# Kernel optimization log

Hardware: AMD Instinct MI355X
Metric: run time of the kernel (lower is better)

Reference implementation:

```python
import jax, jax.numpy as jnp
import numpy as np

B, S, D, H = 2, 2048, 1024, 16
HD = D // H  # head dim = 64


def setup_inputs() -> dict:
    key = jax.random.key(0)
    k1, k2, k3, k4 = jax.random.split(key, 4)
    x = jax.random.normal(k1, (B, S, D), dtype=jnp.float32)
    context = jax.random.normal(k2, (B, S, D), dtype=jnp.float32)
    Wq = jax.random.normal(k3, (D, D), dtype=jnp.float32) * 0.02   # to_query weight [out,in]
    Wkv = jax.random.normal(k4, (2 * D, D), dtype=jnp.float32) * 0.02  # to_key_value weight [out,in]
    return {"x": x, "context": context, "Wq": Wq, "Wkv": Wkv}


def reference(x, context, Wq, Wkv):
    b, i, _ = x.shape
    j = context.shape[1]
    # projections (torch Linear: y = x @ W.T)
    q = x @ Wq.T                      # [b, i, D]
    kv = context @ Wkv.T              # [b, j, 2D]
    k, v = kv[..., :D], kv[..., D:]
    # split heads: (h c) ordering -> reshape last dim to [H, HD]
    q = q.reshape(b, i, H, HD).transpose(0, 2, 1, 3)  # [b,h,i,c]
    k = k.reshape(b, j, H, HD).transpose(0, 2, 1, 3)  # [b,h,j,c]
    v = v.reshape(b, j, H, HD).transpose(0, 2, 1, 3)  # [b,h,j,c]
    q = q * (HD ** -0.5)
    scores = jnp.einsum('bhic,bhjc->bhij', q, k)      # [b,h,i,j]
    scores = scores - jax.lax.stop_gradient(scores.max(axis=-1, keepdims=True))
    attn = jax.nn.softmax(scores, axis=-1)
    out = jnp.einsum('bhij,bhjc->bhic', attn, v)      # [b,h,i,c]
    out = out.transpose(0, 2, 1, 3).reshape(b, i, H * HD)  # 'b h n d -> b n (h d)'
    return out
```

## Files before the change

### kernel.cpp

```cpp
#include <hip/hip_runtime.h>
#include <hip/hip_bf16.h>
#include <stdint.h>

typedef unsigned short u16;
typedef __attribute__((ext_vector_type(8))) __bf16 bf16x8;
typedef __attribute__((ext_vector_type(4))) float f32x4;
typedef __attribute__((ext_vector_type(16))) float f32x16;

#define AS1(p) ((const __attribute__((address_space(1))) void*)(p))
#define AS3(p) ((__attribute__((address_space(3))) void*)(p))

__device__ __forceinline__ u16 f2bf(float f) {
  union { float f; uint32_t u; } c; c.f = f;
  uint32_t u = c.u;
  u += 0x7fffu + ((u >> 16) & 1u);
  return (u16)(u >> 16);
}

__device__ __forceinline__ float exp2_fast(float x) {
  float r; asm("v_exp_f32 %0, %1" : "=v"(r) : "v"(x)); return r;
}

__global__ __launch_bounds__(256) void cast4_f32_bf16(
    const float4* __restrict__ s0, ushort4* __restrict__ d0, int n0,
    const float4* __restrict__ s1, ushort4* __restrict__ d1, int n1,
    const float4* __restrict__ s2, ushort4* __restrict__ d2, int n2,
    const float4* __restrict__ s3, ushort4* __restrict__ d3, int n3) {
  int bid = blockIdx.x;
  const float4* src; ushort4* dst; int n4, b0, nb;
  if (bid < 512)       { src = s0; dst = d0; n4 = n0; b0 = 0;    nb = 512; }
  else if (bid < 1024) { src = s1; dst = d1; n4 = n1; b0 = 512;  nb = 512; }
  else if (bid < 1152) { src = s2; dst = d2; n4 = n2; b0 = 1024; nb = 128; }
  else                 { src = s3; dst = d3; n4 = n3; b0 = 1152; nb = 256; }
  int stride = nb * 256;
  for (int i = (bid - b0) * 256 + threadIdx.x; i < n4; i += stride) {
    float4 v = src[i];
    ushort4 o;
    o.x = f2bf(v.x); o.y = f2bf(v.y); o.z = f2bf(v.z); o.w = f2bf(v.w);
    dst[i] = o;
  }
}

__global__ __launch_bounds__(256) void gemm_fused(const u16* __restrict__ xb,
                                                  const u16* __restrict__ wqb,
                                                  u16* __restrict__ qo,
                                                  const u16* __restrict__ cb,
                                                  const u16* __restrict__ wkb,
                                                  u16* __restrict__ kvo,
                                                  float scale_q) {
  __shared__ u16 As[2][128 * 32];
  __shared__ u16 Bs[2][128 * 32];
  const int K = 1024;
  int bid = blockIdx.x;
  const u16 *A, *B; u16* C; int N, bm, bn; float scale;
  if (bid < 256) { A = xb; B = wqb; C = qo;  N = 1024; bm = bid >> 3; bn = bid & 7;  scale = scale_q; }
  else { int b2 = bid - 256; A = cb; B = wkb; C = kvo; N = 2048; bm = b2 >> 4; bn = b2 & 15; scale = 1.0f; }

  int tid = threadIdx.x;
  int w = tid >> 6, l = tid & 63;
  int wr = w >> 1, wc = w & 1;
  int lr = l & 15, lg = l >> 4;

  const u16* Abase = A + (size_t)(bm * 128 + (l >> 2)) * K + (l & 3) * 8;
  const u16* Bbase = B + (size_t)(bn * 128 + (l >> 2)) * K + (l & 3) * 8;

  f32x4 acc[4][4];
#pragma unroll
  for (int i = 0; i < 4; ++i)
#pragma unroll
    for (int j = 0; j < 4; ++j) acc[i][j] = (f32x4){0.f, 0.f, 0.f, 0.f};

#define STAGE(buf, k0)                                                              \
  {                                                                                 \
    _Pragma("unroll")                                                               \
    for (int t2 = 0; t2 < 2; ++t2) {                                                \
      int seg = w * 2 + t2;                                                         \
      __builtin_amdgcn_global_load_lds(AS1(Abase + (size_t)seg * 16 * K + (k0)),    \
                                       AS3(&As[buf][seg * 512]), 16, 0, 0);         \
      __builtin_amdgcn_global_load_lds(AS1(Bbase + (size_t)seg * 16 * K + (k0)),    \
                                       AS3(&Bs[buf][seg * 512]), 16, 0, 0);         \
    }                                                                               \
  }

  STAGE(0, 0);
  for (int t = 0; t < 32; ++t) {
    int cur = t & 1;
    if (t < 31) {
      STAGE(cur ^ 1, (t + 1) * 32);
      asm volatile("s_waitcnt vmcnt(4)" ::: "memory");
    } else {
      asm volatile("s_waitcnt vmcnt(0)" ::: "memory");
    }
    __builtin_amdgcn_s_barrier();
    bf16x8 af[4], bb[4];
#pragma unroll
    for (int i = 0; i < 4; ++i)
      af[i] = *(const bf16x8*)(&As[cur][(wr * 64 + i * 16 + lr) * 32 + lg * 8]);
#pragma unroll
    for (int j = 0; j < 4; ++j)
      bb[j] = *(const bf16x8*)(&Bs[cur][(wc * 64 + j * 16 + lr) * 32 + lg * 8]);
    asm volatile("s_waitcnt lgkmcnt(0)" ::: "memory");
    __builtin_amdgcn_sched_barrier(0);
#pragma unroll
    for (int i = 0; i < 4; ++i)
#pragma unroll
      for (int j = 0; j < 4; ++j)
        acc[i][j] = __builtin_amdgcn_mfma_f32_16x16x32_bf16(af[i], bb[j], acc[i][j], 0, 0, 0);
    __builtin_amdgcn_s_barrier();
  }
#undef STAGE

#pragma unroll
  for (int i = 0; i < 4; ++i)
#pragma unroll
    for (int j = 0; j < 4; ++j)
#pragma unroll
      for (int r = 0; r < 4; ++r) {
        int row = bm * 128 + wr * 64 + i * 16 + lg * 4 + r;
        int col = bn * 128 + wc * 64 + j * 16 + lr;
        C[(size_t)row * N + col] = f2bf(acc[i][j][r] * scale);
      }
}

#define SQ 2048
#define NT 32

__global__ __launch_bounds__(256, 2) void attn_kernel(const u16* __restrict__ Q,
                                                      const u16* __restrict__ KV,
                                                      float* __restrict__ O) {
  __shared__ u16 Ks[2 * 64 * 64];
  __shared__ u16 Vt[2 * 64 * 64];

  int qt = blockIdx.x & 15;
  int bh = blockIdx.x >> 4;
  int b = bh >> 4, h = bh & 15;
  int tid = threadIdx.x;
  int w = tid >> 6, l = tid & 63;
  int li = l & 31, hi = l >> 5;
  int jr = l >> 3, bk = l & 7;

  const u16* kbase = KV + (size_t)b * SQ * 2048 + (size_t)h * 64;
  const u16* vbase = kbase + 1024;
  int i0g = qt * 128 + w * 32;
  const u16* qrow = Q + (size_t)(b * SQ + i0g + li) * 1024 + h * 64;

  bf16x8 qf0 = *(const bf16x8*)(qrow + 0  + hi * 8);
  bf16x8 qf1 = *(const bf16x8*)(qrow + 16 + hi * 8);
  bf16x8 qf2 = *(const bf16x8*)(qrow + 32 + hi * 8);
  bf16x8 qf3 = *(const bf16x8*)(qrow + 48 + hi * 8);

  {
    const u16* gk0 = kbase + (size_t)(w * 8 + jr) * 2048 + ((bk ^ jr) * 8);
    __builtin_amdgcn_global_load_lds(AS1(gk0), AS3(Ks + w * 512), 16, 0, 0);
    const u16* gk1 = kbase + (size_t)(32 + w * 8 + jr) * 2048 + ((bk ^ jr) * 8);
    __builtin_amdgcn_global_load_lds(AS1(gk1), AS3(Ks + 2048 + w * 512), 16, 0, 0);
  }
  uint4 vregA = *(const uint4*)(vbase + (size_t)(tid >> 3) * 2048 + (tid & 7) * 8);
  uint4 vregB = *(const uint4*)(vbase + (size_t)(32 + (tid >> 3)) * 2048 + (tid & 7) * 8);

  float m_run = -1e30f, l_run = 0.f;
  f32x16 acc0, acc1;
#pragma unroll
  for (int r = 0; r < 16; ++r) { acc0[r] = 0.f; acc1[r] = 0.f; }

  auto stage_pf = [&](int t) {
    u16* Vtc = Vt + (t & 1) * 4096;
    int a = tid & 7, jj0 = tid >> 3;
    const u16* pa_ = (const u16*)&vregA;
#pragma unroll
    for (int e = 0; e < 8; ++e)
      *(u16*)((char*)Vtc + (a * 8 + e) * 128 + ((jj0 * 2) ^ ((e ^ a) << 4))) = pa_[e];
    const u16* pb_ = (const u16*)&vregB;
    int jj1 = 32 + jj0;
#pragma unroll
    for (int e = 0; e < 8; ++e)
      *(u16*)((char*)Vtc + (a * 8 + e) * 128 + ((jj1 * 2) ^ ((e ^ a) << 4))) = pb_[e];
    if (t + 1 < NT) {
      int j0n = (t + 1) * 64;
      u16* Ksn = Ks + ((t + 1) & 1) * 4096;
      const u16* gk0 = kbase + (size_t)(j0n + w * 8 + jr) * 2048 + ((bk ^ jr) * 8);
      __builtin_amdgcn_global_load_lds(AS1(gk0), AS3(Ksn + w * 512), 16, 0, 0);
      const u16* gk1 = kbase + (size_t)(j0n + 32 + w * 8 + jr) * 2048 + ((bk ^ jr) * 8);
      __builtin_amdgcn_global_load_lds(AS1(gk1), AS3(Ksn + 2048 + w * 512), 16, 0, 0);
      vregA = *(const uint4*)(vbase + (size_t)(j0n + (tid >> 3)) * 2048 + (tid & 7) * 8);
      vregB = *(const uint4*)(vbase + (size_t)(j0n + 32 + (tid >> 3)) * 2048 + (tid & 7) * 8);
    }
  };

  auto qkt = [&](int t, f32x16& n0, f32x16& n1) {
    const u16* Ksc = Ks + (t & 1) * 4096;
#pragma unroll
    for (int r = 0; r < 16; ++r) { n0[r] = 0.f; n1[r] = 0.f; }
    int swk = (li & 7) << 4;
    __builtin_amdgcn_s_setprio(1);
#pragma unroll
    for (int kb = 0; kb < 4; ++kb) {
      bf16x8 k0 = *(const bf16x8*)((const char*)Ksc + li * 128        + ((kb * 32 + hi * 16) ^ swk));
      bf16x8 k1 = *(const bf16x8*)((const char*)Ksc + (32 + li) * 128 + ((kb * 32 + hi * 16) ^ swk));
      bf16x8 qq = (kb == 0) ? qf0 : (kb == 1) ? qf1 : (kb == 2) ? qf2 : qf3;
      n0 = __builtin_amdgcn_mfma_f32_32x32x16_bf16(k0, qq, n0, 0, 0, 0);
      n1 = __builtin_amdgcn_mfma_f32_32x32x16_bf16(k1, qq, n1, 0, 0, 0);
    }
    __builtin_amdgcn_s_setprio(0);
  };

  auto finish_pv = [&](int tp, const f32x16& sp0, const f32x16& sp1) {
    const u16* Vtp = Vt + (tp & 1) * 4096;
    float p0[16], p1[16];
    float sum = 0.f;
#pragma unroll
    for (int r = 0; r < 16; ++r) { p0[r] = exp2_fast(sp0[r] - m_run); sum += p0[r]; }
#pragma unroll
    for (int r = 0; r < 16; ++r) { p1[r] = exp2_fast(sp1[r] - m_run); sum += p1[r]; }
    sum += __shfl_xor(sum, 32);
    l_run += sum;
    unsigned pw[16];
#pragma unroll
    for (int i2 = 0; i2 < 8; ++i2) {
      asm("v_cvt_pk_bf16_f32 %0, %1, %2" : "=v"(pw[i2])     : "v"(p0[2 * i2]), "v"(p0[2 * i2 + 1]));
      asm("v_cvt_pk_bf16_f32 %0, %1, %2" : "=v"(pw[8 + i2]) : "v"(p1[2 * i2]), "v"(p1[2 * i2 + 1]));
    }
#pragma unroll
    for (int gB = 0; gB < 2; ++gB) {
      int o = gB * 8;
      asm volatile("v_permlane32_swap_b32 %0, %1" : "+v"(pw[o + 0]), "+v"(pw[o + 2]));
      asm volatile("v_permlane32_swap_b32 %0, %1" : "+v"(pw[o + 1]), "+v"(pw[o + 3]));
      asm volatile("v_permlane32_swap_b32 %0, %1" : "+v"(pw[o + 4]), "+v"(pw[o + 6]));
      asm volatile("v_permlane32_swap_b32 %0, %1" : "+v"(pw[o + 5]), "+v"(pw[o + 7]));
    }
    __builtin_amdgcn_s_setprio(1);
#pragma unroll
    for (int kb2 = 0; kb2 < 4; ++kb2) {
      uint4 ufr;
      ufr.x = pw[kb2 * 4 + 0]; ufr.y = pw[kb2 * 4 + 1];
      ufr.z = pw[kb2 * 4 + 2]; ufr.w = pw[kb2 * 4 + 3];
      bf16x8 pa = *(bf16x8*)&ufr;
      int jbyte = kb2 * 32 + hi * 16;
      int d0_ = li, d1_ = 32 + li;
      bf16x8 v0 = *(const bf16x8*)((const char*)Vtp + d0_ * 128 + (jbyte ^ (((d0_ ^ (d0_ >> 3)) & 7) << 4)));
      bf16x8 v1 = *(const bf16x8*)((const char*)Vtp + d1_ * 128 + (jbyte ^ (((d1_ ^ (d1_ >> 3)) & 7) << 4)));
      acc0 = __builtin_amdgcn_mfma_f32_32x32x16_bf16(v0, pa, acc0, 0, 0, 0);
      acc1 = __builtin_amdgcn_mfma_f32_32x32x16_bf16(v1, pa, acc1, 0, 0, 0);
    }
    __builtin_amdgcn_s_setprio(0);
  };

  auto maxred = [&](const f32x16& n0, const f32x16& n1) {
    float pm = fmaxf(n0[0], n0[1]);
#pragma unroll
    for (int r = 2; r < 16; r += 2) pm = fmaxf(fmaxf(pm, n0[r]), n0[r + 1]);
#pragma unroll
    for (int r = 0; r < 16; r += 2) pm = fmaxf(fmaxf(pm, n1[r]), n1[r + 1]);
    pm = fmaxf(pm, __shfl_xor(pm, 32));
    if (!__all(pm <= m_run + 8.0f)) {
      float mnew = fmaxf(m_run, pm);
      float esc = exp2_fast(m_run - mnew);
      m_run = mnew;
      l_run *= esc;
#pragma unroll
      for (int r = 0; r < 16; ++r) { acc0[r] *= esc; acc1[r] *= esc; }
    }
  };

  f32x16 sa0, sa1, sb0, sb1;
  __syncthreads();
  stage_pf(0);
  qkt(0, sa0, sa1);
  maxred(sa0, sa1);
  for (int t = 1; t < NT - 1; t += 2) {
    __syncthreads();
    stage_pf(t);
    qkt(t, sb0, sb1);
    finish_pv(t - 1, sa0, sa1);
    maxred(sb0, sb1);
    __syncthreads();
    stage_pf(t + 1);
    qkt(t + 1, sa0, sa1);
    finish_pv(t, sb0, sb1);
    maxred(sa0, sa1);
  }
  __syncthreads();
  stage_pf(NT - 1);
  qkt(NT - 1, sb0, sb1);
  finish_pv(NT - 2, sa0, sa1);
  maxred(sb0, sb1);
  __syncthreads();
  finish_pv(NT - 1, sb0, sb1);

  float inv = 1.f / l_run;
  float* orow = O + ((size_t)(b * SQ + i0g + li) * 1024 + h * 64);
#pragma unroll
  for (int g = 0; g < 4; ++g) {
    f32x4 o0, o1;
#pragma unroll
    for (int q_ = 0; q_ < 4; ++q_) {
      o0[q_] = acc0[g * 4 + q_] * inv;
      o1[q_] = acc1[g * 4 + q_] * inv;
    }
    *(f32x4*)(orow + 8 * g + 4 * hi) = o0;
    *(f32x4*)(orow + 32 + 8 * g + 4 * hi) = o1;
  }
}

extern "C" void kernel_launch(void* const* d_in, const int* in_sizes, int n_in,
                              void* d_out, int out_size, void* d_ws, size_t ws_size,
                              hipStream_t stream) {
  (void)in_sizes; (void)n_in; (void)out_size; (void)ws_size;
  const float* x   = (const float*)d_in[0];
  const float* ctx = (const float*)d_in[1];
  const float* Wq  = (const float*)d_in[2];
  const float* Wkv = (const float*)d_in[3];
  float* out = (float*)d_out;
  char* ws = (char*)d_ws;

  u16* xb  = (u16*)(ws);
  u16* cb  = (u16*)(ws + (8ull  << 20));
  u16* wqb = (u16*)(ws + (16ull << 20));
  u16* wkb = (u16*)(ws + (18ull << 20));
  u16* q   = (u16*)(ws + (22ull << 20));
  u16* kv  = (u16*)(ws + (30ull << 20));

  cast4_f32_bf16<<<1408, 256, 0, stream>>>(
      (const float4*)x,   (ushort4*)xb,  (4096 * 1024) / 4,
      (const float4*)ctx, (ushort4*)cb,  (4096 * 1024) / 4,
      (const float4*)Wq,  (ushort4*)wqb, (1024 * 1024) / 4,
      (const float4*)Wkv, (ushort4*)wkb, (2048 * 1024) / 4);

  gemm_fused<<<768, 256, 0, stream>>>(xb, wqb, q, cb, wkb, kv, 0.125f * 1.44269504f);

  attn_kernel<<<512, 256, 0, stream>>>(q, kv, out);
}
```

Before: 110.9 us.

## Fuse fp32-to-bf16 cast into projection GEMM and drop the cast kernel

Removes the separate cast kernel. The GEMM now loads fp32 activations and weights directly into registers, converts them with packed bf16 conversion instructions and writes them to a swizzled LDS layout. The next tile is prefetched in registers instead of using async global-to-LDS loads. This saves one launch and a write/read round trip of the bf16 copies. In exchange each GEMM tile reads twice the bytes, and weights are reconverted in every block, with register pressure raised by the occupancy hint of 3.

```diff
diff --git a/kernel.cpp b/kernel.cpp
--- a/kernel.cpp
+++ b/kernel.cpp
@@ -21,48 +21,36 @@
   float r; asm("v_exp_f32 %0, %1" : "=v"(r) : "v"(x)); return r;
 }
 
-__global__ __launch_bounds__(256) void cast4_f32_bf16(
-    const float4* __restrict__ s0, ushort4* __restrict__ d0, int n0,
-    const float4* __restrict__ s1, ushort4* __restrict__ d1, int n1,
-    const float4* __restrict__ s2, ushort4* __restrict__ d2, int n2,
-    const float4* __restrict__ s3, ushort4* __restrict__ d3, int n3) {
-  int bid = blockIdx.x;
-  const float4* src; ushort4* dst; int n4, b0, nb;
-  if (bid < 512)       { src = s0; dst = d0; n4 = n0; b0 = 0;    nb = 512; }
-  else if (bid < 1024) { src = s1; dst = d1; n4 = n1; b0 = 512;  nb = 512; }
-  else if (bid < 1152) { src = s2; dst = d2; n4 = n2; b0 = 1024; nb = 128; }
-  else                 { src = s3; dst = d3; n4 = n3; b0 = 1152; nb = 256; }
-  int stride = nb * 256;
-  for (int i = (bid - b0) * 256 + threadIdx.x; i < n4; i += stride) {
-    float4 v = src[i];
-    ushort4 o;
-    o.x = f2bf(v.x); o.y = f2bf(v.y); o.z = f2bf(v.z); o.w = f2bf(v.w);
-    dst[i] = o;
-  }
-}
-
-__global__ __launch_bounds__(256) void gemm_fused(const u16* __restrict__ xb,
-                                                  const u16* __restrict__ wqb,
-                                                  u16* __restrict__ qo,
-                                                  const u16* __restrict__ cb,
-                                                  const u16* __restrict__ wkb,
-                                                  u16* __restrict__ kvo,
-                                                  float scale_q) {
+__device__ __forceinline__ unsigned pkbf(float lo, float hi) {
+  unsigned r;
+  asm("v_cvt_pk_bf16_f32 %0, %1, %2" : "=v"(r) : "v"(lo), "v"(hi));
+  return r;
+}
+
+__global__ __launch_bounds__(256, 3) void gemm_fused(const float* __restrict__ xf,
+                                                     const float* __restrict__ wqf,
+                                                     u16* __restrict__ qo,
+                                                     const float* __restrict__ cf,
+                                                     const float* __restrict__ wkf,
+                                                     u16* __restrict__ kvo,
+                                                     float scale_q) {
   __shared__ u16 As[2][128 * 32];
   __shared__ u16 Bs[2][128 * 32];
   const int K = 1024;
   int bid = blockIdx.x;
-  const u16 *A, *B; u16* C; int N, bm, bn; float scale;
-  if (bid < 256) { A = xb; B = wqb; C = qo;  N = 1024; bm = bid >> 3; bn = bid & 7;  scale = scale_q; }
-  else { int b2 = bid - 256; A = cb; B = wkb; C = kvo; N = 2048; bm = b2 >> 4; bn = b2 & 15; scale = 1.0f; }
+  const float *A, *B; u16* C; int N, bm, bn; float scale;
+  if (bid < 256) { A = xf; B = wqf; C = qo;  N = 1024; bm = bid >> 3; bn = bid & 7;  scale = scale_q; }
+  else { int b2 = bid - 256; A = cf; B = wkf; C = kvo; N = 2048; bm = b2 >> 4; bn = b2 & 15; scale = 1.0f; }
 
   int tid = threadIdx.x;
   int w = tid >> 6, l = tid & 63;
   int wr = w >> 1, wc = w & 1;
   int lr = l & 15, lg = l >> 4;
 
-  const u16* Abase = A + (size_t)(bm * 128 + (l >> 2)) * K + (l & 3) * 8;
-  const u16* Bbase = B + (size_t)(bn * 128 + (l >> 2)) * K + (l & 3) * 8;
+  int ra = tid >> 1, ca = tid & 1;
+  const float* Ag = A + (size_t)(bm * 128 + ra) * K + ca * 16;
+  const float* Bg = B + (size_t)(bn * 128 + ra) * K + ca * 16;
+  int swz8 = ((ra >> 1) & 3) << 3;
 
   f32x4 acc[4][4];
 #pragma unroll
@@ -70,35 +58,47 @@
 #pragma unroll
     for (int j = 0; j < 4; ++j) acc[i][j] = (f32x4){0.f, 0.f, 0.f, 0.f};
 
-#define STAGE(buf, k0)                                                              \
-  {                                                                                 \
-    _Pragma("unroll")                                                               \
-    for (int t2 = 0; t2 < 2; ++t2) {                                                \
-      int seg = w * 2 + t2;                                                         \
-      __builtin_amdgcn_global_load_lds(AS1(Abase + (size_t)seg * 16 * K + (k0)),    \
-                                       AS3(&As[buf][seg * 512]), 16, 0, 0);         \
-      __builtin_amdgcn_global_load_lds(AS1(Bbase + (size_t)seg * 16 * K + (k0)),    \
-                                       AS3(&Bs[buf][seg * 512]), 16, 0, 0);         \
-    }                                                                               \
-  }
-
-  STAGE(0, 0);
+  float4 a0 = *(const float4*)(Ag + 0),  a1 = *(const float4*)(Ag + 4);
+  float4 a2 = *(const float4*)(Ag + 8),  a3 = *(const float4*)(Ag + 12);
+  float4 b0 = *(const float4*)(Bg + 0),  b1 = *(const float4*)(Bg + 4);
+  float4 b2 = *(const float4*)(Bg + 8),  b3 = *(const float4*)(Bg + 12);
+
   for (int t = 0; t < 32; ++t) {
     int cur = t & 1;
+    uint4 pA0, pA1, pB0, pB1;
+    pA0.x = pkbf(a0.x, a0.y); pA0.y = pkbf(a0.z, a0.w);
+    pA0.z = pkbf(a1.x, a1.y); pA0.w = pkbf(a1.z, a1.w);
+    pA1.x = pkbf(a2.x, a2.y); pA1.y = pkbf(a2.z, a2.w);
+    pA1.z = pkbf(a3.x, a3.y); pA1.w = pkbf(a3.z, a3.w);
+    pB0.x = pkbf(b0.x, b0.y); pB0.y = pkbf(b0.z, b0.w);
+    pB0.z = pkbf(b1.x, b1.y); pB0.w = pkbf(b1.z, b1.w);
+    pB1.x = pkbf(b2.x, b2.y); pB1.y = pkbf(b2.z, b2.w);
+    pB1.z = pkbf(b3.x, b3.y); pB1.w = pkbf(b3.z, b3.w);
+    *(uint4*)(&As[cur][ra * 32 + ((ca * 16 + 0) ^ swz8)]) = pA0;
+    *(uint4*)(&As[cur][ra * 32 + ((ca * 16 + 8) ^ swz8)]) = pA1;
+    *(uint4*)(&Bs[cur][ra * 32 + ((ca * 16 + 0) ^ swz8)]) = pB0;
+    *(uint4*)(&Bs[cur][ra * 32 + ((ca * 16 + 8) ^ swz8)]) = pB1;
     if (t < 31) {
-      STAGE(cur ^ 1, (t + 1) * 32);
-      asm volatile("s_waitcnt vmcnt(4)" ::: "memory");
-    } else {
-      asm volatile("s_waitcnt vmcnt(0)" ::: "memory");
-    }
+      const float* An = Ag + (t + 1) * 32;
+      const float* Bn = Bg + (t + 1) * 32;
+      a0 = *(const float4*)(An + 0);  a1 = *(const float4*)(An + 4);
+      a2 = *(const float4*)(An + 8);  a3 = *(const float4*)(An + 12);
+      b0 = *(const float4*)(Bn + 0);  b1 = *(const float4*)(Bn + 4);
+      b2 = *(const float4*)(Bn + 8);  b3 = *(const float4*)(Bn + 12);
+    }
+    asm volatile("s_waitcnt lgkmcnt(0)" ::: "memory");
     __builtin_amdgcn_s_barrier();
     bf16x8 af[4], bb[4];
 #pragma unroll
-    for (int i = 0; i < 4; ++i)
-      af[i] = *(const bf16x8*)(&As[cur][(wr * 64 + i * 16 + lr) * 32 + lg * 8]);
-#pragma unroll
-    for (int j = 0; j < 4; ++j)
-      bb[j] = *(const bf16x8*)(&Bs[cur][(wc * 64 + j * 16 + lr) * 32 + lg * 8]);
+    for (int i = 0; i < 4; ++i) {
+      int row = wr * 64 + i * 16 + lr;
+      af[i] = *(const bf16x8*)(&As[cur][row * 32 + ((lg * 8) ^ (((row >> 1) & 3) << 3))]);
+    }
+#pragma unroll
+    for (int j = 0; j < 4; ++j) {
+      int row = wc * 64 + j * 16 + lr;
+      bb[j] = *(const bf16x8*)(&Bs[cur][row * 32 + ((lg * 8) ^ (((row >> 1) & 3) << 3))]);
+    }
     asm volatile("s_waitcnt lgkmcnt(0)" ::: "memory");
     __builtin_amdgcn_sched_barrier(0);
 #pragma unroll
@@ -108,7 +108,6 @@
         acc[i][j] = __builtin_amdgcn_mfma_f32_16x16x32_bf16(af[i], bb[j], acc[i][j], 0, 0, 0);
     __builtin_amdgcn_s_barrier();
   }
-#undef STAGE
 
 #pragma unroll
   for (int i = 0; i < 4; ++i)
@@ -313,20 +312,10 @@
   float* out = (float*)d_out;
   char* ws = (char*)d_ws;
 
-  u16* xb  = (u16*)(ws);
-  u16* cb  = (u16*)(ws + (8ull  << 20));
-  u16* wqb = (u16*)(ws + (16ull << 20));
-  u16* wkb = (u16*)(ws + (18ull << 20));
-  u16* q   = (u16*)(ws + (22ull << 20));
-  u16* kv  = (u16*)(ws + (30ull << 20));
-
-  cast4_f32_bf16<<<1408, 256, 0, stream>>>(
-      (const float4*)x,   (ushort4*)xb,  (4096 * 1024) / 4,
-      (const float4*)ctx, (ushort4*)cb,  (4096 * 1024) / 4,
-      (const float4*)Wq,  (ushort4*)wqb, (1024 * 1024) / 4,
-      (const float4*)Wkv, (ushort4*)wkb, (2048 * 1024) / 4);
-
-  gemm_fused<<<768, 256, 0, stream>>>(xb, wqb, q, cb, wkb, kv, 0.125f * 1.44269504f);
+  u16* q  = (u16*)(ws);
+  u16* kv = (u16*)(ws + (8ull << 20));
+
+  gemm_fused<<<768, 256, 0, stream>>>(x, Wq, q, ctx, Wkv, kv, 0.125f * 1.44269504f);
 
   attn_kernel<<<512, 256, 0, stream>>>(q, kv, out);
 }
```

Result: slower. 116.7 us (+5.2%).
